# Performance work log

Hardware: AMD Instinct MI355X
Metric: run time of the kernel (lower is better)

## Reference

```python
import math
import jax, jax.numpy as jnp
import numpy as np

B, S, T, D, H, L, V, MID = 4, 512, 512, 512, 8, 4, 32000, 2048
MAXLEN = 5000


def make_pos_emb():
    den = jnp.exp(-jnp.arange(0, D, 2, dtype=jnp.float32) * math.log(10000.0) / D)
    pos = jnp.arange(MAXLEN, dtype=jnp.float32)[:, None]
    pe = jnp.zeros((MAXLEN, D), jnp.float32)
    pe = pe.at[:, 0::2].set(jnp.sin(pos * den))
    pe = pe.at[:, 1::2].set(jnp.cos(pos * den))
    return pe[:, None, :]  # (MAXLEN, 1, D), matches unsqueeze(-2)


def setup_inputs() -> dict:
    key = jax.random.key(0)
    ks = list(jax.random.split(key, 12))
    w = lambda k, sh: jax.random.normal(k, sh, jnp.float32) * 0.02
    return {
        "src_words": jax.random.randint(ks[0], (B, S), 0, V),
        "target_words": jax.random.normal(ks[1], (B, T, D), jnp.float32),
        "src_mask": jnp.ones((B, 1, 1, S), jnp.int32),
        "target_mask": jnp.ones((B, 1, T, T), jnp.int32),
        "emb": w(ks[2], (V, D)),
        "pos_emb": make_pos_emb(),
        "enc_ln_g": jnp.ones((L, D)), "enc_ln_b": jnp.zeros((L, D)),
        "enc_attn_w": w(ks[3], (L, 4, D, D)), "enc_attn_b": jnp.zeros((L, 4, D)),
        "enc_fc1_w": w(ks[4], (L, MID, D)), "enc_fc1_b": jnp.zeros((L, MID)),
        "enc_fc2_w": w(ks[5], (L, D, MID)), "enc_fc2_b": jnp.zeros((L, D)),
        "dec_ln_g": jnp.ones((L, D)), "dec_ln_b": jnp.zeros((L, D)),
        "dec_self_w": w(ks[6], (L, 4, D, D)), "dec_self_b": jnp.zeros((L, 4, D)),
        "dec_src_w": w(ks[7], (L, 4, D, D)), "dec_src_b": jnp.zeros((L, 4, D)),
        "dec_fc1_w": w(ks[8], (L, MID, D)), "dec_fc1_b": jnp.zeros((L, MID)),
        "dec_fc2_w": w(ks[9], (L, D, MID)), "dec_fc2_b": jnp.zeros((L, D)),
    }


def _ln(x, g, b):
    mu = jnp.mean(x, -1, keepdims=True)
    var = jnp.mean((x - mu) ** 2, -1, keepdims=True)
    return (x - mu) * jax.lax.rsqrt(var + 1e-5) * g + b


def _mha(q_in, k_in, v_in, W, bias, mask):
    # Faithful to source: view(B, H, -1, d_k) is a plain reshape (NO transpose).
    dk = D // H
    lin = lambda x, i: jnp.einsum('bsd,ed->bse', x, W[i]) + bias[i]
    q = lin(q_in, 0).reshape(q_in.shape[0], H, -1, dk)
    k = lin(k_in, 1).reshape(k_in.shape[0], H, -1, dk)
    v = lin(v_in, 2).reshape(v_in.shape[0], H, -1, dk)
    scores = jnp.einsum('bhqd,bhkd->bhqk', q, k) / jnp.sqrt(jnp.float32(dk))
    if mask is not None:
        scores = jnp.where(mask == 0, jnp.finfo(scores.dtype).min, scores)
    wts = jax.nn.softmax(scores, axis=-1)
    ctx = jnp.einsum('bhqk,bhkd->bhqd', wts, v)
    ctx = jnp.transpose(ctx, (0, 2, 1, 3)).reshape(q_in.shape[0], -1, D)
    return jnp.einsum('bsd,ed->bse', ctx, W[3]) + bias[3]


def _ffn(x, w1, b1, w2, b2):
    h = jax.nn.relu(jnp.einsum('bsd,md->bsm', x, w1) + b1)
    return jnp.einsum('bsm,dm->bsd', h, w2) + b2


def _forward(src_words, target_words, src_mask, target_mask, emb, pos_emb,
             enc_ln_g, enc_ln_b, enc_attn_w, enc_attn_b, enc_fc1_w, enc_fc1_b,
             enc_fc2_w, enc_fc2_b, dec_ln_g, dec_ln_b, dec_self_w, dec_self_b,
             dec_src_w, dec_src_b, dec_fc1_w, dec_fc1_b, dec_fc2_w, dec_fc2_b):
    # Faithful: pos_embedding sliced by tokens.size(0) == batch dim (source quirk).
    x = emb[src_words] + pos_emb[:src_words.shape[0]]
    for i in range(L):
        a = _ln(_mha(x, x, x, enc_attn_w[i], enc_attn_b[i], src_mask) + x,
                enc_ln_g[i], enc_ln_b[i])
        x = _ln(_ffn(a, enc_fc1_w[i], enc_fc1_b[i], enc_fc2_w[i], enc_fc2_b[i]) + a,
                enc_ln_g[i], enc_ln_b[i])
    y = target_words  # source passes target_words raw into decode (no embedding)
    for i in range(L):
        q = _ln(_mha(y, y, y, dec_self_w[i], dec_self_b[i], target_mask) + y,
                dec_ln_g[i], dec_ln_b[i])
        inter = _ln(_mha(q, x, x, dec_src_w[i], dec_src_b[i], None) + q,
                    dec_ln_g[i], dec_ln_b[i])
        y = _ln(_ffn(inter, dec_fc1_w[i], dec_fc1_b[i], dec_fc2_w[i], dec_fc2_b[i]) + inter,
                dec_ln_g[i], dec_ln_b[i])
    return y


def reference(src_words, target_words, src_mask, target_mask, emb, pos_emb,
              enc_ln_g, enc_ln_b, enc_attn_w, enc_attn_b, enc_fc1_w, enc_fc1_b,
              enc_fc2_w, enc_fc2_b, dec_ln_g, dec_ln_b, dec_self_w, dec_self_b,
              dec_src_w, dec_src_b, dec_fc1_w, dec_fc1_b, dec_fc2_w, dec_fc2_b):
    return _forward(src_words, target_words, src_mask, target_mask, emb, pos_emb,
                    enc_ln_g, enc_ln_b, enc_attn_w, enc_attn_b, enc_fc1_w, enc_fc1_b,
                    enc_fc2_w, enc_fc2_b, dec_ln_g, dec_ln_b, dec_self_w, dec_self_b,
                    dec_src_w, dec_src_b, dec_fc1_w, dec_fc1_b, dec_fc2_w, dec_fc2_b)
```

## Files before the change

kernel.cpp:

```cpp
#include <hip/hip_runtime.h>

typedef __attribute__((ext_vector_type(4))) float f32x4;
typedef __attribute__((ext_vector_type(8))) short bf16x8;

#define NB 4
#define NS 512
#define ND 512
#define NH 8
#define NMID 2048
#define DDW (ND*ND)
#define SLAB 32768
#define BSD (NS*ND)

__device__ __forceinline__ unsigned short f2bf_rne(float f) {
    unsigned u = __float_as_uint(f);
    unsigned r = u + 0x7FFFu + ((u >> 16) & 1u);
    return (unsigned short)(r >> 16);
}

__device__ __forceinline__ float wave_sum(float v) {
#pragma unroll
    for (int off = 32; off; off >>= 1) v += __shfl_xor(v, off, 64);
    return v;
}
__device__ __forceinline__ float wave_max(float v) {
#pragma unroll
    for (int off = 32; off; off >>= 1) v = fmaxf(v, __shfl_xor(v, off, 64));
    return v;
}

__global__ __launch_bounds__(256) void embed_k(const int* __restrict__ toks,
                                               const float* __restrict__ emb,
                                               const float* __restrict__ pos,
                                               float* __restrict__ x) {
    int idx = blockIdx.x * 256 + threadIdx.x;
    int d4 = idx & 127;
    int s  = (idx >> 7) & 511;
    int b  = idx >> 16;
    int tok = toks[b * NS + s];
    f32x4 e = *(const f32x4*)(emb + (long)tok * ND + d4 * 4);
    f32x4 p = *(const f32x4*)(pos + (long)b * ND + d4 * 4);
    *(f32x4*)(x + (long)idx * 4) = e + p;
}

__global__ __launch_bounds__(256) void add_ln_k(const float* __restrict__ a,
                                                const float* __restrict__ b,
                                                const float* __restrict__ g,
                                                const float* __restrict__ bb,
                                                float* __restrict__ o) {
    int r = blockIdx.x * 4 + (threadIdx.x >> 6);
    int lane = threadIdx.x & 63;
    const float* pa = a + (long)r * ND + lane * 8;
    const float* pb = b + (long)r * ND + lane * 8;
    f32x4 va0 = *(const f32x4*)pa, va1 = *(const f32x4*)(pa + 4);
    f32x4 vb0 = *(const f32x4*)pb, vb1 = *(const f32x4*)(pb + 4);
    float v[8];
#pragma unroll
    for (int j = 0; j < 4; ++j) { v[j] = va0[j] + vb0[j]; v[4 + j] = va1[j] + vb1[j]; }
    float s = 0.f;
#pragma unroll
    for (int j = 0; j < 8; ++j) s += v[j];
    float mu = wave_sum(s) * (1.0f / 512.0f);
    float vs = 0.f;
#pragma unroll
    for (int j = 0; j < 8; ++j) { float d = v[j] - mu; vs += d * d; }
    float rs = rsqrtf(wave_sum(vs) * (1.0f / 512.0f) + 1e-5f);
    const float* gp = g + lane * 8; const float* bp = bb + lane * 8;
    f32x4 g0 = *(const f32x4*)gp, g1 = *(const f32x4*)(gp + 4);
    f32x4 b0 = *(const f32x4*)bp, b1 = *(const f32x4*)(bp + 4);
    f32x4 o0, o1;
#pragma unroll
    for (int j = 0; j < 4; ++j) {
        o0[j] = (v[j] - mu) * rs * g0[j] + b0[j];
        o1[j] = (v[4 + j] - mu) * rs * g1[j] + b1[j];
    }
    float* po = o + (long)r * ND + lane * 8;
    *(f32x4*)po = o0; *(f32x4*)(po + 4) = o1;
}

template <int MODE>
__global__ __launch_bounds__(256) void softmax_rows(float* __restrict__ sc,
                                                    const int* __restrict__ mask) {
    int r = blockIdx.x * 4 + (threadIdx.x >> 6);
    int lane = threadIdx.x & 63;
    float* row = sc + (long)r * 512;
    int b = r >> 12;
    int q = r & 511;
    f32x4 v0 = *(f32x4*)(row + lane * 8);
    f32x4 v1 = *(f32x4*)(row + lane * 8 + 4);
    float v[8];
#pragma unroll
    for (int j = 0; j < 4; ++j) { v[j] = v0[j]; v[4 + j] = v1[j]; }
    if (MODE == 1) {
        const int* mp = mask + (long)b * 512 + lane * 8;
#pragma unroll
        for (int j = 0; j < 8; ++j) if (mp[j] == 0) v[j] = -3.4e38f;
    }
    if (MODE == 2) {
        const int* mp = mask + (long)b * 512 * 512 + (long)q * 512 + lane * 8;
#pragma unroll
        for (int j = 0; j < 8; ++j) if (mp[j] == 0) v[j] = -3.4e38f;
    }
    float mx = -3.4e38f;
#pragma unroll
    for (int j = 0; j < 8; ++j) mx = fmaxf(mx, v[j]);
    mx = wave_max(mx);
    float s = 0.f;
#pragma unroll
    for (int j = 0; j < 8; ++j) { v[j] = __expf(v[j] - mx); s += v[j]; }
    float inv = 1.0f / wave_sum(s);
#pragma unroll
    for (int j = 0; j < 4; ++j) { v0[j] = v[j] * inv; v1[j] = v[4 + j] * inv; }
    *(f32x4*)(row + lane * 8) = v0;
    *(f32x4*)(row + lane * 8 + 4) = v1;
}

__global__ __launch_bounds__(256) void transpose_v(const float* __restrict__ vb,
                                                   float* __restrict__ vt) {
    int z = blockIdx.x;
    int s2t = blockIdx.y;
    __shared__ float tile[64][65];
    const float* src = vb + (long)z * SLAB + (long)s2t * 64 * 64;
    int tid = threadIdx.x;
#pragma unroll
    for (int it = 0; it < 16; ++it) {
        int idx = it * 256 + tid;
        int s2l = idx >> 6, j = idx & 63;
        tile[j][s2l] = src[idx];
    }
    __syncthreads();
    float* dst = vt + (long)z * SLAB + s2t * 64;
#pragma unroll
    for (int it = 0; it < 16; ++it) {
        int idx = it * 256 + tid;
        int jl = idx >> 6, s2l = idx & 63;
        dst[(long)jl * 512 + s2l] = tile[jl][s2l];
    }
}

template <int ROWS>
__device__ __forceinline__ void stage_tile(const float* __restrict__ src, int ld,
                                           unsigned short* hi, unsigned short* lo,
                                           int tid) {
    constexpr int ITER = ROWS / 16;
#pragma unroll
    for (int i = 0; i < ITER; ++i) {
        int idx = i * 256 + tid;
        int row = idx >> 4, c4 = idx & 15;
        f32x4 v = *(const f32x4*)(src + (long)row * ld + c4 * 4);
        unsigned long long hp = 0ull, lp = 0ull;
#pragma unroll
        for (int j = 0; j < 4; ++j) {
            unsigned u = __float_as_uint(v[j]);
            float hf = __uint_as_float(u & 0xFFFF0000u);
            unsigned short hbits = (unsigned short)(u >> 16);
            unsigned short lbits = f2bf_rne(v[j] - hf);
            hp |= (unsigned long long)hbits << (16 * j);
            lp |= (unsigned long long)lbits << (16 * j);
        }
        int byteoff = row * 128 + ((c4 * 8) ^ ((row & 7) << 4));
        *(unsigned long long*)((char*)hi + byteoff) = hp;
        *(unsigned long long*)((char*)lo + byteoff) = lp;
    }
}

__device__ __forceinline__ bf16x8 ld_frag(const unsigned short* base, int row, int kbyte) {
    int byteoff = row * 128 + (kbyte ^ ((row & 7) << 4));
    return *(const bf16x8*)((const char*)base + byteoff);
}

template <int BM, int BN, bool RELU>
__global__ __launch_bounds__(256, 2) void gemm_split(
    const float* __restrict__ A, const float* __restrict__ W,
    const float* __restrict__ bias, float* __restrict__ C,
    int K, int lda, int ldw, int ldc, float alpha,
    long aZ, long wZ, long cZb, long cZh, int batch_h,
    int colMod, long colBuf) {
    constexpr int FR = BM / 32, FC = BN / 32;
    __shared__ unsigned short Ah[BM * 64], Al[BM * 64], Bh[BN * 64], Bl[BN * 64];
    int tid = threadIdx.x;
    int z = blockIdx.z;
    int zb = z / batch_h, zh = z - zb * batch_h;
    const float* Ap = A + (long)z * aZ + (long)blockIdx.x * BM * lda;
    int bn0 = blockIdx.y * BN;
    const float* Wp = W + (long)z * wZ + (long)bn0 * ldw;
    float* Cp = C + (long)zb * cZb + (long)zh * cZh + (long)blockIdx.x * BM * ldc;
    int colbase = bn0;
    if (colMod) { int which = bn0 / colMod; Cp += (long)which * colBuf; colbase = bn0 - which * colMod; }

    f32x4 acc[FR][FC];
#pragma unroll
    for (int i = 0; i < FR; ++i)
#pragma unroll
        for (int j = 0; j < FC; ++j) acc[i][j] = (f32x4){0.f, 0.f, 0.f, 0.f};

    int wv = tid >> 6, lane = tid & 63;
    int wr = (wv >> 1) * (BM / 2), wc = (wv & 1) * (BN / 2);
    int lrow = lane & 15, lkb = (lane >> 4) * 16;

    for (int kt = 0; kt < K; kt += 64) {
        __syncthreads();
        stage_tile<BM>(Ap + kt, lda, Ah, Al, tid);
        stage_tile<BN>(Wp + kt, ldw, Bh, Bl, tid);
        __syncthreads();
#pragma unroll
        for (int kk = 0; kk < 2; ++kk) {
            int kb = kk * 64 + lkb;
            bf16x8 ah[FR], al[FR], bh[FC], bl[FC];
#pragma unroll
            for (int i = 0; i < FR; ++i) {
                int rr = wr + i * 16 + lrow;
                ah[i] = ld_frag(Ah, rr, kb);
                al[i] = ld_frag(Al, rr, kb);
            }
#pragma unroll
            for (int j = 0; j < FC; ++j) {
                int cc = wc + j * 16 + lrow;
                bh[j] = ld_frag(Bh, cc, kb);
                bl[j] = ld_frag(Bl, cc, kb);
            }
#pragma unroll
            for (int i = 0; i < FR; ++i)
#pragma unroll
                for (int j = 0; j < FC; ++j) {
                    acc[i][j] = __builtin_amdgcn_mfma_f32_16x16x32_bf16(ah[i], bh[j], acc[i][j], 0, 0, 0);
                    acc[i][j] = __builtin_amdgcn_mfma_f32_16x16x32_bf16(ah[i], bl[j], acc[i][j], 0, 0, 0);
                    acc[i][j] = __builtin_amdgcn_mfma_f32_16x16x32_bf16(al[i], bh[j], acc[i][j], 0, 0, 0);
                }
        }
    }
#pragma unroll
    for (int i = 0; i < FR; ++i) {
        int rowl = wr + i * 16 + (lane >> 4) * 4;
#pragma unroll
        for (int j = 0; j < FC; ++j) {
            int coll = wc + j * 16 + lrow;
            float bv = bias ? bias[bn0 + coll] : 0.0f;
#pragma unroll
            for (int r = 0; r < 4; ++r) {
                float v = acc[i][j][r] * alpha + bv;
                if (RELU) v = fmaxf(v, 0.0f);
                Cp[(long)(rowl + r) * ldc + colbase + coll] = v;
            }
        }
    }
}

template <int BM, int BN, bool RELU>
static inline void launch_gemm(hipStream_t st, const float* A, const float* W,
                               const float* bias, float* C, int M, int N, int K,
                               int lda, int ldw, int ldc, float alpha,
                               long aZ, long wZ, long cZb, long cZh, int bh,
                               int colMod, long colBuf, int nz) {
    dim3 grid(M / BM, N / BN, nz);
    gemm_split<BM, BN, RELU><<<grid, 256, 0, st>>>(A, W, bias, C, K, lda, ldw, ldc,
                                                   alpha, aZ, wZ, cZb, cZh, bh, colMod, colBuf);
}

extern "C" void kernel_launch(void* const* d_in, const int* in_sizes, int n_in,
                              void* d_out, int out_size, void* d_ws, size_t ws_size,
                              hipStream_t stream) {
    const int*   src_words    = (const int*)d_in[0];
    const float* target_words = (const float*)d_in[1];
    const int*   src_mask     = (const int*)d_in[2];
    const int*   target_mask  = (const int*)d_in[3];
    const float* emb          = (const float*)d_in[4];
    const float* pos_emb      = (const float*)d_in[5];
    const float* enc_ln_g     = (const float*)d_in[6];
    const float* enc_ln_b     = (const float*)d_in[7];
    const float* enc_attn_w   = (const float*)d_in[8];
    const float* enc_attn_b   = (const float*)d_in[9];
    const float* enc_fc1_w    = (const float*)d_in[10];
    const float* enc_fc1_b    = (const float*)d_in[11];
    const float* enc_fc2_w    = (const float*)d_in[12];
    const float* enc_fc2_b    = (const float*)d_in[13];
    const float* dec_ln_g     = (const float*)d_in[14];
    const float* dec_ln_b     = (const float*)d_in[15];
    const float* dec_self_w   = (const float*)d_in[16];
    const float* dec_self_b   = (const float*)d_in[17];
    const float* dec_src_w    = (const float*)d_in[18];
    const float* dec_src_b    = (const float*)d_in[19];
    const float* dec_fc1_w    = (const float*)d_in[20];
    const float* dec_fc1_b    = (const float*)d_in[21];
    const float* dec_fc2_w    = (const float*)d_in[22];
    const float* dec_fc2_b    = (const float*)d_in[23];
    float* out = (float*)d_out;

    const long M1 = 1 << 20;
    float* ws    = (float*)d_ws;
    float* x_enc = ws;           float* t1  = ws + 1 * M1;  float* t2 = ws + 2 * M1;
    float* t3    = ws + 3 * M1;  float* qb  = ws + 4 * M1;  float* kb = ws + 5 * M1;
    float* vb    = ws + 6 * M1;  float* vt  = ws + 7 * M1;  float* ctx = ws + 8 * M1;
    float* ybuf  = ws + 9 * M1;  float* big = ws + 10 * M1;
    if (ws_size < (size_t)(10 * M1 + 8 * M1) * sizeof(float)) return;

    embed_k<<<1024, 256, 0, stream>>>(src_words, emb, pos_emb, x_enc);

    for (int i = 0; i < 4; ++i) {
        const float* Wl = enc_attn_w + (size_t)i * 4 * DDW;
        const float* bl = enc_attn_b + (size_t)i * 4 * ND;
        const float* g  = enc_ln_g + (size_t)i * ND;
        const float* be = enc_ln_b + (size_t)i * ND;
        launch_gemm<128, 128, false>(stream, x_enc, Wl, bl, qb, 2048, 1536, 512,
                                     512, 512, 512, 1.f, 0, 0, 0, 0, 1, 512, M1, 1);
        transpose_v<<<dim3(32, 8), 256, 0, stream>>>(vb, vt);
        launch_gemm<128, 128, false>(stream, qb, kb, nullptr, big, 512, 512, 64,
                                     64, 64, 512, 0.125f, SLAB, SLAB, BSD, 0, 1, 0, 0, 32);
        softmax_rows<1><<<4096, 256, 0, stream>>>(big, src_mask);
        launch_gemm<64, 64, false>(stream, big, vt, nullptr, ctx, 512, 64, 512,
                                   512, 512, 512, 1.f, BSD, SLAB, BSD, 64, 8, 0, 0, 32);
        launch_gemm<64, 64, false>(stream, ctx, Wl + 3 * DDW, bl + 3 * ND, t1, 2048, 512, 512,
                                   512, 512, 512, 1.f, 0, 0, 0, 0, 1, 0, 0, 1);
        add_ln_k<<<512, 256, 0, stream>>>(t1, x_enc, g, be, t2);
        launch_gemm<128, 128, true>(stream, t2, enc_fc1_w + (size_t)i * NMID * ND,
                                    enc_fc1_b + (size_t)i * NMID, big, 2048, 2048, 512,
                                    512, 512, 2048, 1.f, 0, 0, 0, 0, 1, 0, 0, 1);
        launch_gemm<64, 64, false>(stream, big, enc_fc2_w + (size_t)i * ND * NMID,
                                   enc_fc2_b + (size_t)i * ND, t1, 2048, 512, 2048,
                                   2048, 2048, 512, 1.f, 0, 0, 0, 0, 1, 0, 0, 1);
        add_ln_k<<<512, 256, 0, stream>>>(t1, t2, g, be, x_enc);
    }

    const float* ystate = target_words;
    for (int i = 0; i < 4; ++i) {
        const float* Ws = dec_self_w + (size_t)i * 4 * DDW;
        const float* bs = dec_self_b + (size_t)i * 4 * ND;
        const float* Wx = dec_src_w + (size_t)i * 4 * DDW;
        const float* bx = dec_src_b + (size_t)i * 4 * ND;
        const float* g  = dec_ln_g + (size_t)i * ND;
        const float* be = dec_ln_b + (size_t)i * ND;
        launch_gemm<128, 128, false>(stream, ystate, Ws, bs, qb, 2048, 1536, 512,
                                     512, 512, 512, 1.f, 0, 0, 0, 0, 1, 512, M1, 1);
        transpose_v<<<dim3(32, 8), 256, 0, stream>>>(vb, vt);
        launch_gemm<128, 128, false>(stream, qb, kb, nullptr, big, 512, 512, 64,
                                     64, 64, 512, 0.125f, SLAB, SLAB, BSD, 0, 1, 0, 0, 32);
        softmax_rows<2><<<4096, 256, 0, stream>>>(big, target_mask);
        launch_gemm<64, 64, false>(stream, big, vt, nullptr, ctx, 512, 64, 512,
                                   512, 512, 512, 1.f, BSD, SLAB, BSD, 64, 8, 0, 0, 32);
        launch_gemm<64, 64, false>(stream, ctx, Ws + 3 * DDW, bs + 3 * ND, t1, 2048, 512, 512,
                                   512, 512, 512, 1.f, 0, 0, 0, 0, 1, 0, 0, 1);
        add_ln_k<<<512, 256, 0, stream>>>(t1, ystate, g, be, t2);
        launch_gemm<64, 64, false>(stream, t2, Wx, bx, qb, 2048, 512, 512,
                                   512, 512, 512, 1.f, 0, 0, 0, 0, 1, 0, 0, 1);
        launch_gemm<64, 64, false>(stream, x_enc, Wx + DDW, bx + ND, kb, 2048, 1024, 512,
                                   512, 512, 512, 1.f, 0, 0, 0, 0, 1, 512, M1, 1);
        transpose_v<<<dim3(32, 8), 256, 0, stream>>>(vb, vt);
        launch_gemm<128, 128, false>(stream, qb, kb, nullptr, big, 512, 512, 64,
                                     64, 64, 512, 0.125f, SLAB, SLAB, BSD, 0, 1, 0, 0, 32);
        softmax_rows<0><<<4096, 256, 0, stream>>>(big, nullptr);
        launch_gemm<64, 64, false>(stream, big, vt, nullptr, ctx, 512, 64, 512,
                                   512, 512, 512, 1.f, BSD, SLAB, BSD, 64, 8, 0, 0, 32);
        launch_gemm<64, 64, false>(stream, ctx, Wx + 3 * DDW, bx + 3 * ND, t1, 2048, 512, 512,
                                   512, 512, 512, 1.f, 0, 0, 0, 0, 1, 0, 0, 1);
        add_ln_k<<<512, 256, 0, stream>>>(t1, t2, g, be, t3);
        launch_gemm<128, 128, true>(stream, t3, dec_fc1_w + (size_t)i * NMID * ND,
                                    dec_fc1_b + (size_t)i * NMID, big, 2048, 2048, 512,
                                    512, 512, 2048, 1.f, 0, 0, 0, 0, 1, 0, 0, 1);
        launch_gemm<64, 64, false>(stream, big, dec_fc2_w + (size_t)i * ND * NMID,
                                   dec_fc2_b + (size_t)i * ND, t1, 2048, 512, 2048,
                                   2048, 2048, 512, 1.f, 0, 0, 0, 0, 1, 0, 0, 1);
        add_ln_k<<<512, 256, 0, stream>>>(t1, t3, g, be, (i == 3) ? out : ybuf);
        ystate = ybuf;
    }
}
```

Baseline: 2.043 ms.

## Pre-split activations and weights to bf16 hi/lo and use direct global-to-LDS loads

```diff
diff --git a/kernel.cpp b/kernel.cpp
--- a/kernel.cpp
+++ b/kernel.cpp
@@ -2,20 +2,37 @@
 
 typedef __attribute__((ext_vector_type(4))) float f32x4;
 typedef __attribute__((ext_vector_type(8))) short bf16x8;
+typedef unsigned short u16;
+typedef __attribute__((ext_vector_type(8))) unsigned short u16x8;
 
 #define NB 4
 #define NS 512
 #define ND 512
-#define NH 8
 #define NMID 2048
 #define DDW (ND*ND)
-#define SLAB 32768
-#define BSD (NS*ND)
-
-__device__ __forceinline__ unsigned short f2bf_rne(float f) {
+
+#define OUT_F32 0
+#define OUT_SPLIT 1
+#define OUT_SRELU 2
+#define OUT_QKV 3
+
+typedef const __attribute__((address_space(1))) void GV;
+typedef __attribute__((address_space(3))) void LV;
+
+__device__ __forceinline__ void gl_lds16(const void* g, void* l) {
+    __builtin_amdgcn_global_load_lds((GV*)g, (LV*)l, 16, 0, 0);
+}
+
+__device__ __forceinline__ u16 f2bf_rne(float f) {
     unsigned u = __float_as_uint(f);
     unsigned r = u + 0x7FFFu + ((u >> 16) & 1u);
-    return (unsigned short)(r >> 16);
+    return (u16)(r >> 16);
+}
+__device__ __forceinline__ void split2(float v, u16& h, u16& l) {
+    unsigned u = __float_as_uint(v);
+    h = (u16)(u >> 16);
+    float hf = __uint_as_float(u & 0xFFFF0000u);
+    l = f2bf_rne(v - hf);
 }
 
 __device__ __forceinline__ float wave_sum(float v) {
@@ -27,27 +44,60 @@
 #pragma unroll
     for (int off = 32; off; off >>= 1) v = fmaxf(v, __shfl_xor(v, off, 64));
     return v;
+}
+
+__global__ __launch_bounds__(256) void split_conv(const float* __restrict__ in,
+                                                  u16* __restrict__ hi,
+                                                  u16* __restrict__ lo, int n8) {
+    int t = blockIdx.x * 256 + threadIdx.x;
+    if (t >= n8) return;
+    const f32x4* p = (const f32x4*)(in + (long)t * 8);
+    f32x4 a = p[0], b = p[1];
+    u16x8 H, L;
+#pragma unroll
+    for (int j = 0; j < 4; ++j) {
+        u16 h, l;
+        split2(a[j], h, l); H[j] = h; L[j] = l;
+        split2(b[j], h, l); H[4 + j] = h; L[4 + j] = l;
+    }
+    *(u16x8*)(hi + (long)t * 8) = H;
+    *(u16x8*)(lo + (long)t * 8) = L;
 }
 
 __global__ __launch_bounds__(256) void embed_k(const int* __restrict__ toks,
                                                const float* __restrict__ emb,
                                                const float* __restrict__ pos,
-                                               float* __restrict__ x) {
-    int idx = blockIdx.x * 256 + threadIdx.x;
-    int d4 = idx & 127;
-    int s  = (idx >> 7) & 511;
-    int b  = idx >> 16;
+                                               float* __restrict__ x,
+                                               u16* __restrict__ xh, u16* __restrict__ xl) {
+    int t = blockIdx.x * 256 + threadIdx.x;
+    int d8 = t & 63;
+    int s  = (t >> 6) & 511;
+    int b  = t >> 15;
     int tok = toks[b * NS + s];
-    f32x4 e = *(const f32x4*)(emb + (long)tok * ND + d4 * 4);
-    f32x4 p = *(const f32x4*)(pos + (long)b * ND + d4 * 4);
-    *(f32x4*)(x + (long)idx * 4) = e + p;
+    const float* ep = emb + (long)tok * ND + d8 * 8;
+    const float* pp = pos + (long)b * ND + d8 * 8;
+    f32x4 e0 = *(const f32x4*)ep, e1 = *(const f32x4*)(ep + 4);
+    f32x4 p0 = *(const f32x4*)pp, p1 = *(const f32x4*)(pp + 4);
+    f32x4 v0 = e0 + p0, v1 = e1 + p1;
+    float* xp = x + (long)t * 8;
+    *(f32x4*)xp = v0; *(f32x4*)(xp + 4) = v1;
+    u16x8 H, L;
+#pragma unroll
+    for (int j = 0; j < 4; ++j) {
+        u16 h, l;
+        split2(v0[j], h, l); H[j] = h; L[j] = l;
+        split2(v1[j], h, l); H[4 + j] = h; L[4 + j] = l;
+    }
+    *(u16x8*)(xh + (long)t * 8) = H;
+    *(u16x8*)(xl + (long)t * 8) = L;
 }
 
 __global__ __launch_bounds__(256) void add_ln_k(const float* __restrict__ a,
                                                 const float* __restrict__ b,
                                                 const float* __restrict__ g,
                                                 const float* __restrict__ bb,
-                                                float* __restrict__ o) {
+                                                float* __restrict__ o,
+                                                u16* __restrict__ oh, u16* __restrict__ ol) {
     int r = blockIdx.x * 4 + (threadIdx.x >> 6);
     int lane = threadIdx.x & 63;
     const float* pa = a + (long)r * ND + lane * 8;
@@ -69,22 +119,31 @@
     f32x4 g0 = *(const f32x4*)gp, g1 = *(const f32x4*)(gp + 4);
     f32x4 b0 = *(const f32x4*)bp, b1 = *(const f32x4*)(bp + 4);
     f32x4 o0, o1;
+    u16x8 H, L;
 #pragma unroll
     for (int j = 0; j < 4; ++j) {
-        o0[j] = (v[j] - mu) * rs * g0[j] + b0[j];
-        o1[j] = (v[4 + j] - mu) * rs * g1[j] + b1[j];
+        float x0 = (v[j] - mu) * rs * g0[j] + b0[j];
+        float x1 = (v[4 + j] - mu) * rs * g1[j] + b1[j];
+        o0[j] = x0; o1[j] = x1;
+        u16 h, l;
+        split2(x0, h, l); H[j] = h; L[j] = l;
+        split2(x1, h, l); H[4 + j] = h; L[4 + j] = l;
     }
     float* po = o + (long)r * ND + lane * 8;
     *(f32x4*)po = o0; *(f32x4*)(po + 4) = o1;
+    *(u16x8*)(oh + (long)r * ND + lane * 8) = H;
+    *(u16x8*)(ol + (long)r * ND + lane * 8) = L;
 }
 
 template <int MODE>
 __global__ __launch_bounds__(256) void softmax_rows(float* __restrict__ sc,
-                                                    const int* __restrict__ mask) {
+                                                    const int* __restrict__ mask,
+                                                    int zoff) {
     int r = blockIdx.x * 4 + (threadIdx.x >> 6);
     int lane = threadIdx.x & 63;
     float* row = sc + (long)r * 512;
-    int b = r >> 12;
+    int gslab = zoff + (r >> 9);
+    int b = gslab >> 3;
     int q = r & 511;
     f32x4 v0 = *(f32x4*)(row + lane * 8);
     f32x4 v1 = *(f32x4*)(row + lane * 8 + 4);
@@ -109,84 +168,57 @@
 #pragma unroll
     for (int j = 0; j < 8; ++j) { v[j] = __expf(v[j] - mx); s += v[j]; }
     float inv = 1.0f / wave_sum(s);
-#pragma unroll
-    for (int j = 0; j < 4; ++j) { v0[j] = v[j] * inv; v1[j] = v[4 + j] * inv; }
-    *(f32x4*)(row + lane * 8) = v0;
-    *(f32x4*)(row + lane * 8 + 4) = v1;
-}
-
-__global__ __launch_bounds__(256) void transpose_v(const float* __restrict__ vb,
-                                                   float* __restrict__ vt) {
-    int z = blockIdx.x;
-    int s2t = blockIdx.y;
-    __shared__ float tile[64][65];
-    const float* src = vb + (long)z * SLAB + (long)s2t * 64 * 64;
+    u16x8 H, L;
+#pragma unroll
+    for (int j = 0; j < 8; ++j) {
+        u16 h, l; split2(v[j] * inv, h, l);
+        H[j] = h; L[j] = l;
+    }
+    u16* ru = (u16*)row;
+    *(u16x8*)(ru + lane * 8) = H;
+    *(u16x8*)(ru + 512 + lane * 8) = L;
+}
+
+template <int R>
+__device__ __forceinline__ void stage_bf16(const u16* __restrict__ src, int ld,
+                                           char* ldsT, int tid) {
+    int w = tid >> 6, l = tid & 63;
+    int cc = l & 7, rsub = l >> 3;
+#pragma unroll
+    for (int i = w; i < R / 8; i += 4) {
+        int row = i * 8 + rsub;
+        const u16* g = src + (long)row * ld + ((cc ^ (row & 7)) << 3);
+        gl_lds16(g, ldsT + i * 1024);
+    }
+}
+
+__device__ __forceinline__ bf16x8 ld_frag(const char* base, int row, int kbyte) {
+    return *(const bf16x8*)(base + row * 128 + (kbyte ^ ((row & 7) << 4)));
+}
+
+template <int BM, int BN, int OM>
+__global__ __launch_bounds__(256) void gemm_bs(
+    const u16* __restrict__ Ahi, const u16* __restrict__ Alo, int lda,
+    long aZl, long aZb, long aZh,
+    const u16* __restrict__ Whi, const u16* __restrict__ Wlo, int ldw,
+    long wZb, long wZh,
+    const float* __restrict__ bias, float alpha, int zoff,
+    float* __restrict__ Cf, u16* __restrict__ Chi, u16* __restrict__ Clo,
+    int ldc, long cZl, long cZb, long cZh,
+    u16* __restrict__ Vhi, u16* __restrict__ Vlo, int colOff, int K) {
+    constexpr int FR = BM / 32, FC = BN / 32;
+    __shared__ char lds[(BM + BN) * 256];
+    constexpr int oAl = BM * 128, oBh = 2 * BM * 128, oBl = 2 * BM * 128 + BN * 128;
     int tid = threadIdx.x;
-#pragma unroll
-    for (int it = 0; it < 16; ++it) {
-        int idx = it * 256 + tid;
-        int s2l = idx >> 6, j = idx & 63;
-        tile[j][s2l] = src[idx];
-    }
-    __syncthreads();
-    float* dst = vt + (long)z * SLAB + s2t * 64;
-#pragma unroll
-    for (int it = 0; it < 16; ++it) {
-        int idx = it * 256 + tid;
-        int jl = idx >> 6, s2l = idx & 63;
-        dst[(long)jl * 512 + s2l] = tile[jl][s2l];
-    }
-}
-
-template <int ROWS>
-__device__ __forceinline__ void stage_tile(const float* __restrict__ src, int ld,
-                                           unsigned short* hi, unsigned short* lo,
-                                           int tid) {
-    constexpr int ITER = ROWS / 16;
-#pragma unroll
-    for (int i = 0; i < ITER; ++i) {
-        int idx = i * 256 + tid;
-        int row = idx >> 4, c4 = idx & 15;
-        f32x4 v = *(const f32x4*)(src + (long)row * ld + c4 * 4);
-        unsigned long long hp = 0ull, lp = 0ull;
-#pragma unroll
-        for (int j = 0; j < 4; ++j) {
-            unsigned u = __float_as_uint(v[j]);
-            float hf = __uint_as_float(u & 0xFFFF0000u);
-            unsigned short hbits = (unsigned short)(u >> 16);
-            unsigned short lbits = f2bf_rne(v[j] - hf);
-            hp |= (unsigned long long)hbits << (16 * j);
-            lp |= (unsigned long long)lbits << (16 * j);
-        }
-        int byteoff = row * 128 + ((c4 * 8) ^ ((row & 7) << 4));
-        *(unsigned long long*)((char*)hi + byteoff) = hp;
-        *(unsigned long long*)((char*)lo + byteoff) = lp;
-    }
-}
-
-__device__ __forceinline__ bf16x8 ld_frag(const unsigned short* base, int row, int kbyte) {
-    int byteoff = row * 128 + (kbyte ^ ((row & 7) << 4));
-    return *(const bf16x8*)((const char*)base + byteoff);
-}
-
-template <int BM, int BN, bool RELU>
-__global__ __launch_bounds__(256, 2) void gemm_split(
-    const float* __restrict__ A, const float* __restrict__ W,
-    const float* __restrict__ bias, float* __restrict__ C,
-    int K, int lda, int ldw, int ldc, float alpha,
-    long aZ, long wZ, long cZb, long cZh, int batch_h,
-    int colMod, long colBuf) {
-    constexpr int FR = BM / 32, FC = BN / 32;
-    __shared__ unsigned short Ah[BM * 64], Al[BM * 64], Bh[BN * 64], Bl[BN * 64];
-    int tid = threadIdx.x;
-    int z = blockIdx.z;
-    int zb = z / batch_h, zh = z - zb * batch_h;
-    const float* Ap = A + (long)z * aZ + (long)blockIdx.x * BM * lda;
+    int z = blockIdx.z, gz = z + zoff;
+    long zb = gz >> 3, zh = gz & 7;
+    long aoff = (long)z * aZl + zb * aZb + zh * aZh + (long)blockIdx.x * BM * lda;
+    const u16* Ah_p = Ahi + aoff;
+    const u16* Al_p = Alo + aoff;
     int bn0 = blockIdx.y * BN;
-    const float* Wp = W + (long)z * wZ + (long)bn0 * ldw;
-    float* Cp = C + (long)zb * cZb + (long)zh * cZh + (long)blockIdx.x * BM * ldc;
-    int colbase = bn0;
-    if (colMod) { int which = bn0 / colMod; Cp += (long)which * colBuf; colbase = bn0 - which * colMod; }
+    long woff = zb * wZb + zh * wZh + (long)bn0 * ldw;
+    const u16* Wh_p = Whi + woff;
+    const u16* Wl_p = Wlo + woff;
 
     f32x4 acc[FR][FC];
 #pragma unroll
@@ -200,8 +232,10 @@
 
     for (int kt = 0; kt < K; kt += 64) {
         __syncthreads();
-        stage_tile<BM>(Ap + kt, lda, Ah, Al, tid);
-        stage_tile<BN>(Wp + kt, ldw, Bh, Bl, tid);
+        stage_bf16<BM>(Ah_p + kt, lda, lds, tid);
+        stage_bf16<BM>(Al_p + kt, lda, lds + oAl, tid);
+        stage_bf16<BN>(Wh_p + kt, ldw, lds + oBh, tid);
+        stage_bf16<BN>(Wl_p + kt, ldw, lds + oBl, tid);
         __syncthreads();
 #pragma unroll
         for (int kk = 0; kk < 2; ++kk) {
@@ -210,14 +244,14 @@
 #pragma unroll
             for (int i = 0; i < FR; ++i) {
                 int rr = wr + i * 16 + lrow;
-                ah[i] = ld_frag(Ah, rr, kb);
-                al[i] = ld_frag(Al, rr, kb);
+                ah[i] = ld_frag(lds, rr, kb);
+                al[i] = ld_frag(lds + oAl, rr, kb);
             }
 #pragma unroll
             for (int j = 0; j < FC; ++j) {
                 int cc = wc + j * 16 + lrow;
-                bh[j] = ld_frag(Bh, cc, kb);
-                bl[j] = ld_frag(Bl, cc, kb);
+                bh[j] = ld_frag(lds + oBh, cc, kb);
+                bl[j] = ld_frag(lds + oBl, cc, kb);
             }
 #pragma unroll
             for (int i = 0; i < FR; ++i)
@@ -229,32 +263,47 @@
                 }
         }
     }
+
+    long crow0 = (long)blockIdx.x * BM;
+    long coffC = (long)z * cZl + zb * cZb + zh * cZh;
 #pragma unroll
     for (int i = 0; i < FR; ++i) {
         int rowl = wr + i * 16 + (lane >> 4) * 4;
 #pragma unroll
         for (int j = 0; j < FC; ++j) {
             int coll = wc + j * 16 + lrow;
-            float bv = bias ? bias[bn0 + coll] : 0.0f;
+            int gc = colOff + bn0 + coll;
+            float bv = bias ? bias[gc] : 0.0f;
 #pragma unroll
             for (int r = 0; r < 4; ++r) {
                 float v = acc[i][j][r] * alpha + bv;
-                if (RELU) v = fmaxf(v, 0.0f);
-                Cp[(long)(rowl + r) * ldc + colbase + coll] = v;
+                long row = crow0 + rowl + r;
+                if constexpr (OM == OUT_F32) {
+                    Cf[coffC + row * ldc + bn0 + coll] = v;
+                } else if constexpr (OM == OUT_SPLIT || OM == OUT_SRELU) {
+                    if constexpr (OM == OUT_SRELU) v = fmaxf(v, 0.0f);
+                    u16 h, l; split2(v, h, l);
+                    long o = coffC + row * ldc + bn0 + coll;
+                    Chi[o] = h; Clo[o] = l;
+                } else {
+                    u16 h, l; split2(v, h, l);
+                    int buf = gc >> 9;
+                    if (buf < 2) {
+                        long o = (long)buf * 1048576 + row * ldc + (gc & 511);
+                        Chi[o] = h; Clo[o] = l;
+                    } else {
+                        int c2 = gc - 1024;
+                        int bq = (int)(row >> 9), ss = (int)(row & 511);
+                        int hq = ss >> 6;
+                        int ii = (ss & 63) * 8 + (c2 >> 6);
+                        int jj = c2 & 63;
+                        long o = ((long)(bq * 8 + hq)) * 32768 + (long)jj * 512 + ii;
+                        Vhi[o] = h; Vlo[o] = l;
+                    }
+                }
             }
         }
     }
-}
-
-template <int BM, int BN, bool RELU>
-static inline void launch_gemm(hipStream_t st, const float* A, const float* W,
-                               const float* bias, float* C, int M, int N, int K,
-                               int lda, int ldw, int ldc, float alpha,
-                               long aZ, long wZ, long cZb, long cZh, int bh,
-                               int colMod, long colBuf, int nz) {
-    dim3 grid(M / BM, N / BN, nz);
-    gemm_split<BM, BN, RELU><<<grid, 256, 0, st>>>(A, W, bias, C, K, lda, ldw, ldc,
-                                                   alpha, aZ, wZ, cZb, cZh, bh, colMod, colBuf);
 }
 
 extern "C" void kernel_launch(void* const* d_in, const int* in_sizes, int n_in,
@@ -286,42 +335,91 @@
     const float* dec_fc2_b    = (const float*)d_in[23];
     float* out = (float*)d_out;
 
-    const long M1 = 1 << 20;
-    float* ws    = (float*)d_ws;
-    float* x_enc = ws;           float* t1  = ws + 1 * M1;  float* t2 = ws + 2 * M1;
-    float* t3    = ws + 3 * M1;  float* qb  = ws + 4 * M1;  float* kb = ws + 5 * M1;
-    float* vb    = ws + 6 * M1;  float* vt  = ws + 7 * M1;  float* ctx = ws + 8 * M1;
-    float* ybuf  = ws + 9 * M1;  float* big = ws + 10 * M1;
-    if (ws_size < (size_t)(10 * M1 + 8 * M1) * sizeof(float)) return;
-
-    embed_k<<<1024, 256, 0, stream>>>(src_words, emb, pos_emb, x_enc);
+    const size_t Mi = 1u << 20;
+    char* W = (char*)d_ws;
+    int nchunk;
+    if (ws_size >= 80 * Mi) nchunk = 1;
+    else if (ws_size >= 64 * Mi) nchunk = 2;
+    else return;
+
+    float* x_enc = (float*)(W + 0);
+    float* t1    = (float*)(W + 4 * Mi);
+    float* t2    = (float*)(W + 8 * Mi);
+    float* ybuf  = (float*)(W + 12 * Mi);
+    u16* xs_h  = (u16*)(W + 16 * Mi); u16* xs_l  = (u16*)(W + 18 * Mi);
+    u16* t2s_h = (u16*)(W + 20 * Mi); u16* t2s_l = (u16*)(W + 22 * Mi);
+    u16* t3s_h = (u16*)(W + 24 * Mi); u16* t3s_l = (u16*)(W + 26 * Mi);
+    u16* qk_h  = (u16*)(W + 28 * Mi);
+    u16* qk_l  = (u16*)(W + 32 * Mi);
+    u16* vt_h  = (u16*)(W + 36 * Mi); u16* vt_l  = (u16*)(W + 38 * Mi);
+    u16* cx_h  = (u16*)(W + 40 * Mi); u16* cx_l  = (u16*)(W + 42 * Mi);
+    u16* w_h   = (u16*)(W + 44 * Mi); u16* w_l   = (u16*)(W + 46 * Mi);
+    char* region = W + 48 * Mi;
+    u16* hs_h = (u16*)region;
+    u16* hs_l = (u16*)(region + 8 * Mi);
+    float* t3 = x_enc;
+    u16 *ys_h = t2s_h, *ys_l = t2s_l;
+
+    auto conv = [&](const float* src, int n) {
+        int n8 = n / 8;
+        split_conv<<<dim3((n8 + 255) / 256), 256, 0, stream>>>(src, w_h, w_l, n8);
+    };
+    auto attention = [&](int mode, const int* mask) {
+        int ns = 32 / nchunk;
+        for (int c = 0; c < nchunk; ++c) {
+            int zoff = c * ns;
+            gemm_bs<64, 64, OUT_F32><<<dim3(8, 8, ns), 256, 0, stream>>>(
+                qk_h, qk_l, 64, 0, 262144, 32768,
+                qk_h + 1048576, qk_l + 1048576, 64, 262144, 32768,
+                nullptr, 0.125f, zoff,
+                (float*)region, nullptr, nullptr, 512, 262144, 0, 0,
+                nullptr, nullptr, 0, 64);
+            if (mode == 0) softmax_rows<0><<<dim3(ns * 128), 256, 0, stream>>>((float*)region, nullptr, zoff);
+            if (mode == 1) softmax_rows<1><<<dim3(ns * 128), 256, 0, stream>>>((float*)region, mask, zoff);
+            if (mode == 2) softmax_rows<2><<<dim3(ns * 128), 256, 0, stream>>>((float*)region, mask, zoff);
+            gemm_bs<32, 64, OUT_SPLIT><<<dim3(16, 1, ns), 256, 0, stream>>>(
+                (u16*)region, (u16*)region + 512, 1024, 524288, 0, 0,
+                vt_h, vt_l, 512, 262144, 32768,
+                nullptr, 1.0f, zoff,
+                nullptr, cx_h, cx_l, 512, 0, 262144, 64,
+                nullptr, nullptr, 0, 512);
+        }
+    };
+
+    embed_k<<<dim3(512), 256, 0, stream>>>(src_words, emb, pos_emb, x_enc, xs_h, xs_l);
 
     for (int i = 0; i < 4; ++i) {
         const float* Wl = enc_attn_w + (size_t)i * 4 * DDW;
         const float* bl = enc_attn_b + (size_t)i * 4 * ND;
         const float* g  = enc_ln_g + (size_t)i * ND;
         const float* be = enc_ln_b + (size_t)i * ND;
-        launch_gemm<128, 128, false>(stream, x_enc, Wl, bl, qb, 2048, 1536, 512,
-                                     512, 512, 512, 1.f, 0, 0, 0, 0, 1, 512, M1, 1);
-        transpose_v<<<dim3(32, 8), 256, 0, stream>>>(vb, vt);
-        launch_gemm<128, 128, false>(stream, qb, kb, nullptr, big, 512, 512, 64,
-                                     64, 64, 512, 0.125f, SLAB, SLAB, BSD, 0, 1, 0, 0, 32);
-        softmax_rows<1><<<4096, 256, 0, stream>>>(big, src_mask);
-        launch_gemm<64, 64, false>(stream, big, vt, nullptr, ctx, 512, 64, 512,
-                                   512, 512, 512, 1.f, BSD, SLAB, BSD, 64, 8, 0, 0, 32);
-        launch_gemm<64, 64, false>(stream, ctx, Wl + 3 * DDW, bl + 3 * ND, t1, 2048, 512, 512,
-                                   512, 512, 512, 1.f, 0, 0, 0, 0, 1, 0, 0, 1);
-        add_ln_k<<<512, 256, 0, stream>>>(t1, x_enc, g, be, t2);
-        launch_gemm<128, 128, true>(stream, t2, enc_fc1_w + (size_t)i * NMID * ND,
-                                    enc_fc1_b + (size_t)i * NMID, big, 2048, 2048, 512,
-                                    512, 512, 2048, 1.f, 0, 0, 0, 0, 1, 0, 0, 1);
-        launch_gemm<64, 64, false>(stream, big, enc_fc2_w + (size_t)i * ND * NMID,
-                                   enc_fc2_b + (size_t)i * ND, t1, 2048, 512, 2048,
-                                   2048, 2048, 512, 1.f, 0, 0, 0, 0, 1, 0, 0, 1);
-        add_ln_k<<<512, 256, 0, stream>>>(t1, t2, g, be, x_enc);
-    }
-
-    const float* ystate = target_words;
+        conv(Wl, 3 * DDW);
+        gemm_bs<64, 64, OUT_QKV><<<dim3(32, 24, 1), 256, 0, stream>>>(
+            xs_h, xs_l, 512, 0, 0, 0, w_h, w_l, 512, 0, 0,
+            bl, 1.0f, 0, nullptr, qk_h, qk_l, 512, 0, 0, 0,
+            vt_h, vt_l, 0, 512);
+        attention(1, src_mask);
+        conv(Wl + 3 * DDW, DDW);
+        gemm_bs<64, 32, OUT_F32><<<dim3(32, 16, 1), 256, 0, stream>>>(
+            cx_h, cx_l, 512, 0, 0, 0, w_h, w_l, 512, 0, 0,
+            bl + 1536, 1.0f, 0, t1, nullptr, nullptr, 512, 0, 0, 0,
+            nullptr, nullptr, 0, 512);
+        add_ln_k<<<dim3(512), 256, 0, stream>>>(t1, x_enc, g, be, t2, t2s_h, t2s_l);
+        conv(enc_fc1_w + (size_t)i * NMID * ND, NMID * ND);
+        gemm_bs<64, 64, OUT_SRELU><<<dim3(32, 32, 1), 256, 0, stream>>>(
+            t2s_h, t2s_l, 512, 0, 0, 0, w_h, w_l, 512, 0, 0,
+            enc_fc1_b + (size_t)i * NMID, 1.0f, 0,
+            nullptr, hs_h, hs_l, 2048, 0, 0, 0, nullptr, nullptr, 0, 512);
+        conv(enc_fc2_w + (size_t)i * ND * NMID, ND * NMID);
+        gemm_bs<64, 32, OUT_F32><<<dim3(32, 16, 1), 256, 0, stream>>>(
+            hs_h, hs_l, 2048, 0, 0, 0, w_h, w_l, 2048, 0, 0,
+            enc_fc2_b + (size_t)i * ND, 1.0f, 0,
+            t1, nullptr, nullptr, 512, 0, 0, 0, nullptr, nullptr, 0, 2048);
+        add_ln_k<<<dim3(512), 256, 0, stream>>>(t1, t2, g, be, x_enc, xs_h, xs_l);
+    }
+
+    split_conv<<<dim3(512), 256, 0, stream>>>(target_words, ys_h, ys_l, 131072);
+    const float* yres = target_words;
     for (int i = 0; i < 4; ++i) {
         const float* Ws = dec_self_w + (size_t)i * 4 * DDW;
         const float* bs = dec_self_b + (size_t)i * 4 * ND;
@@ -329,37 +427,45 @@
         const float* bx = dec_src_b + (size_t)i * 4 * ND;
         const float* g  = dec_ln_g + (size_t)i * ND;
         const float* be = dec_ln_b + (size_t)i * ND;
-        launch_gemm<128, 128, false>(stream, ystate, Ws, bs, qb, 2048, 1536, 512,
-                                     512, 512, 512, 1.f, 0, 0, 0, 0, 1, 512, M1, 1);
-        transpose_v<<<dim3(32, 8), 256, 0, stream>>>(vb, vt);
-        launch_gemm<128, 128, false>(stream, qb, kb, nullptr, big, 512, 512, 64,
-                                     64, 64, 512, 0.125f, SLAB, SLAB, BSD, 0, 1, 0, 0, 32);
-        softmax_rows<2><<<4096, 256, 0, stream>>>(big, target_mask);
-        launch_gemm<64, 64, false>(stream, big, vt, nullptr, ctx, 512, 64, 512,
-                                   512, 512, 512, 1.f, BSD, SLAB, BSD, 64, 8, 0, 0, 32);
-        launch_gemm<64, 64, false>(stream, ctx, Ws + 3 * DDW, bs + 3 * ND, t1, 2048, 512, 512,
-                                   512, 512, 512, 1.f, 0, 0, 0, 0, 1, 0, 0, 1);
-        add_ln_k<<<512, 256, 0, stream>>>(t1, ystate, g, be, t2);
-        launch_gemm<64, 64, false>(stream, t2, Wx, bx, qb, 2048, 512, 512,
-                                   512, 512, 512, 1.f, 0, 0, 0, 0, 1, 0, 0, 1);
-        launch_gemm<64, 64, false>(stream, x_enc, Wx + DDW, bx + ND, kb, 2048, 1024, 512,
-                                   512, 512, 512, 1.f, 0, 0, 0, 0, 1, 512, M1, 1);
-        transpose_v<<<dim3(32, 8), 256, 0, stream>>>(vb, vt);
-        launch_gemm<128, 128, false>(stream, qb, kb, nullptr, big, 512, 512, 64,
-                                     64, 64, 512, 0.125f, SLAB, SLAB, BSD, 0, 1, 0, 0, 32);
-        softmax_rows<0><<<4096, 256, 0, stream>>>(big, nullptr);
-        launch_gemm<64, 64, false>(stream, big, vt, nullptr, ctx, 512, 64, 512,
-                                   512, 512, 512, 1.f, BSD, SLAB, BSD, 64, 8, 0, 0, 32);
-        launch_gemm<64, 64, false>(stream, ctx, Wx + 3 * DDW, bx + 3 * ND, t1, 2048, 512, 512,
-                                   512, 512, 512, 1.f, 0, 0, 0, 0, 1, 0, 0, 1);
-        add_ln_k<<<512, 256, 0, stream>>>(t1, t2, g, be, t3);
-        launch_gemm<128, 128, true>(stream, t3, dec_fc1_w + (size_t)i * NMID * ND,
-                                    dec_fc1_b + (size_t)i * NMID, big, 2048, 2048, 512,
-                                    512, 512, 2048, 1.f, 0, 0, 0, 0, 1, 0, 0, 1);
-        launch_gemm<64, 64, false>(stream, big, dec_fc2_w + (size_t)i * ND * NMID,
-                                   dec_fc2_b + (size_t)i * ND, t1, 2048, 512, 2048,
-                                   2048, 2048, 512, 1.f, 0, 0, 0, 0, 1, 0, 0, 1);
-        add_ln_k<<<512, 256, 0, stream>>>(t1, t3, g, be, (i == 3) ? out : ybuf);
-        ystate = ybuf;
-    }
-}
+        conv(Ws, 3 * DDW);
+        gemm_bs<64, 64, OUT_QKV><<<dim3(32, 24, 1), 256, 0, stream>>>(
+            ys_h, ys_l, 512, 0, 0, 0, w_h, w_l, 512, 0, 0,
+            bs, 1.0f, 0, nullptr, qk_h, qk_l, 512, 0, 0, 0,
+            vt_h, vt_l, 0, 512);
+        attention(2, target_mask);
+        conv(Ws + 3 * DDW, DDW);
+        gemm_bs<64, 32, OUT_F32><<<dim3(32, 16, 1), 256, 0, stream>>>(
+            cx_h, cx_l, 512, 0, 0, 0, w_h, w_l, 512, 0, 0,
+            bs + 1536, 1.0f, 0, t1, nullptr, nullptr, 512, 0, 0, 0,
+            nullptr, nullptr, 0, 512);
+        add_ln_k<<<dim3(512), 256, 0, stream>>>(t1, yres, g, be, t2, t2s_h, t2s_l);
+        conv(Wx, 3 * DDW);
+        gemm_bs<64, 32, OUT_QKV><<<dim3(32, 16, 1), 256, 0, stream>>>(
+            t2s_h, t2s_l, 512, 0, 0, 0, w_h, w_l, 512, 0, 0,
+            bx, 1.0f, 0, nullptr, qk_h, qk_l, 512, 0, 0, 0,
+            vt_h, vt_l, 0, 512);
+        gemm_bs<64, 64, OUT_QKV><<<dim3(32, 16, 1), 256, 0, stream>>>(
+            xs_h, xs_l, 512, 0, 0, 0, w_h + 512 * 512, w_l + 512 * 512, 512, 0, 0,
+            bx, 1.0f, 0, nullptr, qk_h, qk_l, 512, 0, 0, 0,
+            vt_h, vt_l, 512, 512);
+        attention(0, nullptr);
+        conv(Wx + 3 * DDW, DDW);
+        gemm_bs<64, 32, OUT_F32><<<dim3(32, 16, 1), 256, 0, stream>>>(
+            cx_h, cx_l, 512, 0, 0, 0, w_h, w_l, 512, 0, 0,
+            bx + 1536, 1.0f, 0, t1, nullptr, nullptr, 512, 0, 0, 0,
+            nullptr, nullptr, 0, 512);
+        add_ln_k<<<dim3(512), 256, 0, stream>>>(t1, t2, g, be, t3, t3s_h, t3s_l);
+        conv(dec_fc1_w + (size_t)i * NMID * ND, NMID * ND);
+        gemm_bs<64, 64, OUT_SRELU><<<dim3(32, 32, 1), 256, 0, stream>>>(
+            t3s_h, t3s_l, 512, 0, 0, 0, w_h, w_l, 512, 0, 0,
+            dec_fc1_b + (size_t)i * NMID, 1.0f, 0,
+            nullptr, hs_h, hs_l, 2048, 0, 0, 0, nullptr, nullptr, 0, 512);
+        conv(dec_fc2_w + (size_t)i * ND * NMID, ND * NMID);
+        gemm_bs<64, 32, OUT_F32><<<dim3(32, 16, 1), 256, 0, stream>>>(
+            hs_h, hs_l, 2048, 0, 0, 0, w_h, w_l, 2048, 0, 0,
+            dec_fc2_b + (size_t)i * ND, 1.0f, 0,
+            t1, nullptr, nullptr, 512, 0, 0, 0, nullptr, nullptr, 0, 2048);
+        add_ln_k<<<dim3(512), 256, 0, stream>>>(t1, t3, g, be, (i == 3) ? out : ybuf, ys_h, ys_l);
+        yres = ybuf;
+    }
+}
```

Result: faster. 1.660 ms (-18.7%).
